# Performance work log

Hardware: AMD Instinct MI355X
Metric: run time of the kernel (lower is better)

## Reference

```python
import jax, jax.numpy as jnp
import numpy as np

E = 512   # embed_dim
H = 8     # num_heads
DH = E // H  # head_dim = 64
L = 1024  # tgt_len (language tokens)
S = 1024  # src_len (video/audio tokens)
B = 8     # batch
EPS = 1e-8


def setup_inputs() -> dict:
    key = jax.random.key(0)
    ks = jax.random.split(key, 12)
    xavier = float(np.sqrt(2.0 / (E + E)))
    inp = {
        "query": jax.random.normal(ks[0], (L, B, E), jnp.float32),
        "mod1": jax.random.normal(ks[1], (S, B, E), jnp.float32),
        "mod2": jax.random.normal(ks[2], (S, B, E), jnp.float32),
    }
    wnames = ["Wq", "Wk1", "Wk2", "Wv1", "Wv2", "Wg1", "Wg2", "Wo"]
    for i, n in enumerate(wnames):
        inp[n] = jax.random.normal(ks[3 + i], (E, E), jnp.float32) * xavier
        inp["b" + n[1:]] = jnp.zeros((E,), jnp.float32)
    return inp


def _heads(x):
    # (T, B, E) -> (B*H, T, DH), fairseq-style head split
    T = x.shape[0]
    return x.reshape(T, B * H, DH).transpose(1, 0, 2)


def reference(query, mod1, mod2,
              Wq, bq, Wk1, bk1, Wk2, bk2,
              Wv1, bv1, Wv2, bv2,
              Wg1, bg1, Wg2, bg2, Wo, bo):
    scaling = DH ** -0.5
    q = (query @ Wq.T + bq) * scaling          # (L, B, E)
    k1 = mod1 @ Wk1.T + bk1                    # (S, B, E)
    k2 = mod2 @ Wk2.T + bk2
    # gated values: v_i * sigmoid(gate_i(mod_i)), summed across modalities
    v = ((mod1 @ Wv1.T + bv1) * jax.nn.sigmoid(mod1 @ Wg1.T + bg1)
         + (mod2 @ Wv2.T + bv2) * jax.nn.sigmoid(mod2 @ Wg2.T + bg2))

    qh, k1h, k2h, vh = _heads(q), _heads(k1), _heads(k2), _heads(v)  # (B*H, T, DH)

    # 3x3 Gram determinant scores (computed via GEMMs, no [B,L,S,D] broadcast)
    ll = jnp.sum(qh * qh, -1)[:, :, None]        # (BH, L, 1)
    vv = jnp.sum(k1h * k1h, -1)[:, None, :]      # (BH, 1, S)
    aa = jnp.sum(k2h * k2h, -1)[:, None, :]
    va = jnp.sum(k1h * k2h, -1)[:, None, :]
    lv = jnp.einsum('bld,bsd->bls', qh, k1h)     # (BH, L, S)
    la = jnp.einsum('bld,bsd->bls', qh, k2h)
    det = (ll * (vv * aa - va * va)
           - lv * (lv * aa - la * va)
           + la * (lv * va - la * vv))
    scores = -jnp.sqrt(jnp.clip(det, EPS))       # (BH, L, S)

    attn = jax.nn.softmax(scores, axis=-1)
    out = jnp.einsum('bls,bsd->bld', attn, vh)   # (BH, L, DH)
    out = out.transpose(1, 0, 2).reshape(L, B, E)
    return out @ Wo.T + bo                       # (L, B, E)
```

## Files before the change

### kernel.cpp

```cpp
#include <hip/hip_runtime.h>
#include <math.h>


typedef short bf16x8 __attribute__((ext_vector_type(8)));
typedef float f32x4  __attribute__((ext_vector_type(4)));

#define MFMA16(a,b,c) __builtin_amdgcn_mfma_f32_16x16x32_bf16((a),(b),(c),0,0,0)

static constexpr float LOG2E_F = 1.4426950408889634f;
static constexpr float CBRT_L2E = 1.12994722f;
static constexpr float DEFER_THR = 11.54156033f;
static constexpr float EPS_SCALED = 2.0813689e-8f;

typedef const __attribute__((address_space(1))) unsigned int gas_u32;
typedef __attribute__((address_space(3))) unsigned int las_u32;

__device__ __forceinline__ void gload16(const void* g, void* l){
  __builtin_amdgcn_global_load_lds((gas_u32*)g, (las_u32*)l, 16, 0, 0);
}

__device__ __forceinline__ float b2f(unsigned short s){
  union { unsigned u; float f; } v; v.u = ((unsigned)s) << 16; return v.f;
}
__device__ __forceinline__ unsigned short f2b(float f){
  union { float f; unsigned u; } v; v.f = f;
  unsigned r = v.u + 0x7fffu + ((v.u >> 16) & 1u);
  return (unsigned short)(r >> 16);
}

__global__ __launch_bounds__(256) void cast3_kernel(
    const float* __restrict__ a, const float* __restrict__ b,
    const float* __restrict__ c, unsigned short* __restrict__ hi, int n)
{
  const int y = blockIdx.y;
  const float* src = (y == 0) ? a : ((y == 1) ? b : c);
  unsigned short* h = hi + (size_t)y * n;
  const int n8 = n >> 3;
  int stride = gridDim.x * 256;
  for (int i = blockIdx.x*256 + threadIdx.x; i < n8; i += stride){
    f32x4 v0 = *(const f32x4*)&src[i*8];
    f32x4 v1 = *(const f32x4*)&src[i*8 + 4];
    bf16x8 o;
    #pragma unroll
    for (int j = 0; j < 4; ++j){
      o[j]   = (short)f2b(v0[j]);
      o[j+4] = (short)f2b(v1[j]);
    }
    *(bf16x8*)&h[i*8] = o;
  }
}

__global__ __launch_bounds__(256) void splitW_kernel(
    const float* w0, const float* w1, const float* w2, const float* w3,
    const float* w4, const float* w5, const float* w6, const float* w7,
    unsigned short* __restrict__ hi, unsigned short* __restrict__ lo, int n)
{
  const int y = blockIdx.y;
  const float* src = w0;
  if (y == 1) src = w1; if (y == 2) src = w2; if (y == 3) src = w3;
  if (y == 4) src = w4; if (y == 5) src = w5; if (y == 6) src = w6;
  if (y == 7) src = w7;
  unsigned short* h = hi + (size_t)y * n;
  unsigned short* L = lo + (size_t)y * n;
  int stride = gridDim.x * 256;
  for (int i = blockIdx.x*256 + threadIdx.x; i < n; i += stride){
    float v = src[i];
    unsigned short hh = f2b(v);
    h[i] = hh;
    L[i] = f2b(v - b2f(hh));
  }
}

__global__ __launch_bounds__(256,3) void proj_qk_kernel(
    const unsigned short* __restrict__ xhi,
    const unsigned short* __restrict__ whi, const unsigned short* __restrict__ wlo,
    const float* __restrict__ bq, const float* __restrict__ bk1,
    const float* __restrict__ bk2,
    unsigned short* __restrict__ qh_hi, unsigned short* __restrict__ qh_lo,
    unsigned short* __restrict__ k1h_hi, unsigned short* __restrict__ k1h_lo,
    unsigned short* __restrict__ k2h_hi, unsigned short* __restrict__ k2h_lo)
{
  __shared__ unsigned short smem[2*3*4096];
  const int tid = threadIdx.x, w = tid >> 6, l = tid & 63;
  const int y = blockIdx.y, job = y >> 2;
  const int r0 = blockIdx.x * 128, e0 = (y & 3) * 128;
  const int lrow = l & 15, kg = l >> 4;

  const size_t NXs = (size_t)8192*512, NWs = (size_t)512*512;
  const unsigned short* Ahi = xhi + (size_t)job * NXs;
  const unsigned short* B1  = whi + (size_t)job * NWs;
  const unsigned short* B2  = wlo + (size_t)job * NWs;

  f32x4 acc[4][4];
  #pragma unroll
  for (int m = 0; m < 4; ++m)
    #pragma unroll
    for (int n = 0; n < 4; ++n) acc[m][n] = (f32x4){0.f,0.f,0.f,0.f};

  const int sgsw = ((l & 3) ^ ((l >> 3) & 3)) * 8;
  const int srA = r0 + w*16 + (l >> 2);
  const int srB = e0 + w*16 + (l >> 2);

  auto stage = [&](int buf, int kk){
    const int lb = buf*3*4096 + w*512;
    #pragma unroll
    for (int j = 0; j < 2; ++j){
      const size_t ga = (size_t)(srA + j*64)*512 + kk + sgsw;
      const size_t gb = (size_t)(srB + j*64)*512 + kk + sgsw;
      gload16(&Ahi[ga], &smem[lb + 0    + j*2048]);
      gload16(&B1[gb],  &smem[lb + 4096 + j*2048]);
      gload16(&B2[gb],  &smem[lb + 8192 + j*2048]);
    }
  };

  const int rowA = (w >> 1)*64 + lrow;
  const int rowB = (w & 1)*64 + lrow;
  const int kgs  = (kg ^ ((lrow >> 1) & 3)) * 8;

  auto compute = [&](int buf){
    const int bb = buf*3*4096;
    bf16x8 ah[4];
    #pragma unroll
    for (int m = 0; m < 4; ++m)
      ah[m] = *(const bf16x8*)&smem[bb + (rowA + m*16)*32 + kgs];
    #pragma unroll
    for (int n = 0; n < 4; ++n){
      const int rb = (rowB + n*16)*32 + kgs;
      bf16x8 b1 = *(const bf16x8*)&smem[bb + 4096 + rb];
      bf16x8 b2 = *(const bf16x8*)&smem[bb + 8192 + rb];
      #pragma unroll
      for (int m = 0; m < 4; ++m){
        acc[m][n] = MFMA16(ah[m], b1, acc[m][n]);
        acc[m][n] = MFMA16(ah[m], b2, acc[m][n]);
      }
    }
  };

  stage(0, 0);
  __syncthreads();
  for (int t = 0; t < 16; ++t){
    if (t < 15) stage((t+1) & 1, (t+1)*32);
    compute(t & 1);
    __syncthreads();
  }

  const float* bias = (job == 0) ? bq : ((job == 1) ? bk1 : bk2);
  const float scale = (job == 0) ? 0.125f*CBRT_L2E : CBRT_L2E;
  unsigned short* oH = (job == 0) ? qh_hi : ((job == 1) ? k1h_hi : k2h_hi);
  unsigned short* oL = (job == 0) ? qh_lo : ((job == 1) ? k1h_lo : k2h_lo);
  #pragma unroll
  for (int n = 0; n < 4; ++n){
    const int e = e0 + (w & 1)*64 + n*16 + lrow;
    const float bv = bias[e];
    #pragma unroll
    for (int m = 0; m < 4; ++m){
      #pragma unroll
      for (int q = 0; q < 4; ++q){
        const int r = r0 + (w >> 1)*64 + m*16 + kg*4 + q;
        const float yv = (acc[m][n][q] + bv) * scale;
        const int bh = ((r & 7) << 3) + (e >> 6);
        const size_t off = ((size_t)bh*1024 + (r >> 3))*64 + (e & 63);
        unsigned short hh = f2b(yv);
        oH[off] = hh;
        oL[off] = f2b(yv - b2f(hh));
      }
    }
  }
}

__global__ __launch_bounds__(256,2) void proj_vg_kernel(
    const unsigned short* __restrict__ xhi,
    const unsigned short* __restrict__ whi,
    const float* __restrict__ bv1, const float* __restrict__ bg1,
    const float* __restrict__ bv2, const float* __restrict__ bg2,
    float* __restrict__ vacc1, float* __restrict__ vacc2)
{
  __shared__ unsigned short smem[2*3*4096];
  const int tid = threadIdx.x, w = tid >> 6, l = tid & 63;
  const int y = blockIdx.y, job = 3 + (y >> 2);
  const int r0 = blockIdx.x * 128, e0 = (y & 3) * 128;
  const int lrow = l & 15, kg = l >> 4;

  const size_t NXs = (size_t)8192*512, NWs = (size_t)512*512;
  const unsigned short* Ahi = xhi + (size_t)(job - 2) * NXs;
  const unsigned short* B1  = whi + (size_t)((job == 3) ? 3 : 4) * NWs;
  const unsigned short* B2  = whi + (size_t)((job == 3) ? 5 : 6) * NWs;

  f32x4 acc[4][4], acc2[4][4];
  #pragma unroll
  for (int m = 0; m < 4; ++m)
    #pragma unroll
    for (int n = 0; n < 4; ++n){
      acc[m][n] = (f32x4){0.f,0.f,0.f,0.f};
      acc2[m][n] = (f32x4){0.f,0.f,0.f,0.f};
    }

  const int sgsw = ((l & 3) ^ ((l >> 3) & 3)) * 8;
  const int srA = r0 + w*16 + (l >> 2);
  const int srB = e0 + w*16 + (l >> 2);

  auto stage = [&](int buf, int kk){
    const int lb = buf*3*4096 + w*512;
    #pragma unroll
    for (int j = 0; j < 2; ++j){
      const size_t ga = (size_t)(srA + j*64)*512 + kk + sgsw;
      const size_t gb = (size_t)(srB + j*64)*512 + kk + sgsw;
      gload16(&Ahi[ga], &smem[lb + 0    + j*2048]);
      gload16(&B1[gb],  &smem[lb + 4096 + j*2048]);
      gload16(&B2[gb],  &smem[lb + 8192 + j*2048]);
    }
  };

  const int rowA = (w >> 1)*64 + lrow;
  const int rowB = (w & 1)*64 + lrow;
  const int kgs  = (kg ^ ((lrow >> 1) & 3)) * 8;

  auto compute = [&](int buf){
    const int bb = buf*3*4096;
    bf16x8 ah[4];
    #pragma unroll
    for (int m = 0; m < 4; ++m)
      ah[m] = *(const bf16x8*)&smem[bb + (rowA + m*16)*32 + kgs];
    #pragma unroll
    for (int n = 0; n < 4; ++n){
      const int rb = (rowB + n*16)*32 + kgs;
      bf16x8 b1 = *(const bf16x8*)&smem[bb + 4096 + rb];
      bf16x8 b2 = *(const bf16x8*)&smem[bb + 8192 + rb];
      #pragma unroll
      for (int m = 0; m < 4; ++m){
        acc[m][n]  = MFMA16(ah[m], b1, acc[m][n]);
        acc2[m][n] = MFMA16(ah[m], b2, acc2[m][n]);
      }
    }
  };

  stage(0, 0);
  __syncthreads();
  for (int t = 0; t < 16; ++t){
    if (t < 15) stage((t+1) & 1, (t+1)*32);
    compute(t & 1);
    __syncthreads();
  }

  const float* bvv = (job == 3) ? bv1 : bv2;
  const float* bgg = (job == 3) ? bg1 : bg2;
  float* outF = (job == 3) ? vacc1 : vacc2;
  #pragma unroll
  for (int n = 0; n < 4; ++n){
    const int e = e0 + (w & 1)*64 + n*16 + lrow;
    const float bv = bvv[e], bg_ = bgg[e];
    #pragma unroll
    for (int m = 0; m < 4; ++m){
      #pragma unroll
      for (int q = 0; q < 4; ++q){
        const int r = r0 + (w >> 1)*64 + m*16 + kg*4 + q;
        const float yv = acc[m][n][q] + bv;
        const float yg = acc2[m][n][q] + bg_;
        const float sg = 1.0f / (1.0f + exp2f(-yg * LOG2E_F));
        outF[(size_t)r*512 + e] = yv * sg;
      }
    }
  }
}

__global__ __launch_bounds__(256,2) void gemmout_kernel(
    const unsigned short* __restrict__ Ahi,
    const unsigned short* __restrict__ Bhi, const unsigned short* __restrict__ Blo,
    const float* __restrict__ bias, float* __restrict__ outF)
{
  __shared__ unsigned short smem[2*10240];
  const int tid = threadIdx.x, w = tid >> 6, l = tid & 63;
  const int r0 = blockIdx.x * 64, e0 = blockIdx.y * 128;
  const int lrow = l & 15, kg = l >> 4;

  f32x4 acc[2][4];
  #pragma unroll
  for (int m = 0; m < 2; ++m)
    #pragma unroll
    for (int n = 0; n < 4; ++n) acc[m][n] = (f32x4){0.f,0.f,0.f,0.f};

  const int sgsw = ((l & 3) ^ ((l >> 3) & 3)) * 8;
  const int srA = r0 + w*16 + (l >> 2);
  const int srB = e0 + w*16 + (l >> 2);

  auto stage = [&](int buf, int kk){
    const int lb = buf*10240;
    gload16(&Ahi[(size_t)srA*512 + kk + sgsw], &smem[lb + tid*8]);
    #pragma unroll
    for (int j = 0; j < 2; ++j){
      const size_t gb = (size_t)(srB + j*64)*512 + kk + sgsw;
      gload16(&Bhi[gb], &smem[lb + 2048 + (tid + j*256)*8]);
      gload16(&Blo[gb], &smem[lb + 6144 + (tid + j*256)*8]);
    }
  };

  const int rowA = (w >> 1)*32 + lrow;
  const int rowB = (w & 1)*64 + lrow;
  const int kgs  = (kg ^ ((lrow >> 1) & 3)) * 8;

  auto compute = [&](int buf){
    const int bb = buf*10240;
    bf16x8 ah[2];
    #pragma unroll
    for (int m = 0; m < 2; ++m)
      ah[m] = *(const bf16x8*)&smem[bb + (rowA + m*16)*32 + kgs];
    #pragma unroll
    for (int n = 0; n < 4; ++n){
      const int rb = (rowB + n*16)*32 + kgs;
      bf16x8 bh = *(const bf16x8*)&smem[bb + 2048 + rb];
      bf16x8 bl = *(const bf16x8*)&smem[bb + 6144 + rb];
      #pragma unroll
      for (int m = 0; m < 2; ++m){
        acc[m][n] = MFMA16(ah[m], bh, acc[m][n]);
        acc[m][n] = MFMA16(ah[m], bl, acc[m][n]);
      }
    }
  };

  stage(0, 0);
  __syncthreads();
  for (int t = 0; t < 16; ++t){
    if (t < 15) stage((t+1) & 1, (t+1)*32);
    compute(t & 1);
    __syncthreads();
  }

  #pragma unroll
  for (int n = 0; n < 4; ++n){
    const int e = e0 + (w & 1)*64 + n*16 + lrow;
    const float bv = bias[e];
    #pragma unroll
    for (int m = 0; m < 2; ++m){
      #pragma unroll
      for (int q = 0; q < 4; ++q){
        const int r = r0 + (w >> 1)*32 + m*16 + kg*4 + q;
        outF[(size_t)r*512 + e] = acc[m][n][q] + bv;
      }
    }
  }
}

__global__ __launch_bounds__(256) void norms_kernel(
    const unsigned short* __restrict__ qh, const unsigned short* __restrict__ ql,
    const unsigned short* __restrict__ k1h, const unsigned short* __restrict__ k1l,
    const unsigned short* __restrict__ k2h, const unsigned short* __restrict__ k2l,
    float* __restrict__ ll, f32x4* __restrict__ nrm4)
{
  const int idx = blockIdx.x*256 + threadIdx.x;
  const size_t base = (size_t)idx * 64;
  float sll = 0.f, svv = 0.f, saa = 0.f, sva = 0.f;
  #pragma unroll
  for (int j = 0; j < 8; ++j){
    bf16x8 q_h = *(const bf16x8*)&qh[base + j*8];
    bf16x8 q_l = *(const bf16x8*)&ql[base + j*8];
    bf16x8 a_h = *(const bf16x8*)&k1h[base + j*8];
    bf16x8 a_l = *(const bf16x8*)&k1l[base + j*8];
    bf16x8 c_h = *(const bf16x8*)&k2h[base + j*8];
    bf16x8 c_l = *(const bf16x8*)&k2l[base + j*8];
    #pragma unroll
    for (int i = 0; i < 8; ++i){
      float qv = b2f((unsigned short)q_h[i]) + b2f((unsigned short)q_l[i]);
      float a1 = b2f((unsigned short)a_h[i]) + b2f((unsigned short)a_l[i]);
      float a2 = b2f((unsigned short)c_h[i]) + b2f((unsigned short)c_l[i]);
      sll += qv*qv; svv += a1*a1; saa += a2*a2; sva += a1*a2;
    }
  }
  ll[idx] = sll;
  nrm4[idx] = (f32x4){svv*saa - sva*sva, saa, 2.0f*sva, svv};
}

__global__ __launch_bounds__(256) void vtrans_kernel(
    const float* __restrict__ v1, const float* __restrict__ v2,
    unsigned short* __restrict__ vTh)
{
  __shared__ unsigned short sH[64*64];
  const int bh = blockIdx.y, b = bh >> 3, h = bh & 7;
  const int s0 = blockIdx.x * 64;
  const int tid = threadIdx.x;
  for (int c = tid; c < 1024; c += 256){
    const int i = c >> 4, sl = c & 15;
    const size_t g = ((size_t)(s0 + i)*8 + b)*512 + h*64 + sl*4;
    f32x4 a = *(const f32x4*)&v1[g];
    f32x4 bb = *(const f32x4*)&v2[g];
    #pragma unroll
    for (int e = 0; e < 4; ++e)
      sH[(sl*4 + e)*64 + i] = f2b(a[e] + bb[e]);
  }
  __syncthreads();
  for (int c = tid; c < 512; c += 256){
    const int d = c >> 3, sl = c & 7;
    const size_t g = ((size_t)bh*64 + d)*1024 + s0 + sl*8;
    *(bf16x8*)&vTh[g] = *(const bf16x8*)&sH[d*64 + sl*8];
  }
}

__global__ __launch_bounds__(256,2) void attn_kernel(
    const unsigned short* __restrict__ qhh, const unsigned short* __restrict__ qhl,
    const unsigned short* __restrict__ k1hh, const unsigned short* __restrict__ k1hl,
    const unsigned short* __restrict__ k2hh, const unsigned short* __restrict__ k2hl,
    const unsigned short* __restrict__ vTh,
    const float* __restrict__ llv, const f32x4* __restrict__ nrm4,
    unsigned short* __restrict__ aoHi)
{
  __shared__ unsigned short sK1h[4096];
  __shared__ unsigned short sK1l[4096];
  __shared__ unsigned short sK2h[4096];
  __shared__ unsigned short sK2l[4096];
  __shared__ unsigned short sVh[4096];
  __shared__ unsigned short sPh[8192];
  __shared__ f32x4 sN4[64];

  const int bh = blockIdx.x & 63, l0 = (blockIdx.x >> 6) * 128;
  const int tid = threadIdx.x, w = tid >> 6, lane = tid & 63;
  const int lrow = lane & 15, kg = lane >> 4;

  bf16x8 qfh[2][2], qfl[2][2];
  #pragma unroll
  for (int m = 0; m < 2; ++m){
    const size_t qb = ((size_t)bh*1024 + l0 + w*32 + m*16 + lrow)*64 + kg*8;
    qfh[m][0] = *(const bf16x8*)&qhh[qb];
    qfl[m][0] = *(const bf16x8*)&qhl[qb];
    qfh[m][1] = *(const bf16x8*)&qhh[qb + 32];
    qfl[m][1] = *(const bf16x8*)&qhl[qb + 32];
  }
  float ll_r[2][4];
  #pragma unroll
  for (int m = 0; m < 2; ++m)
    #pragma unroll
    for (int q = 0; q < 4; ++q)
      ll_r[m][q] = llv[bh*1024 + l0 + w*32 + m*16 + kg*4 + q];

  f32x4 accO[2][4];
  #pragma unroll
  for (int m = 0; m < 2; ++m)
    #pragma unroll
    for (int i = 0; i < 4; ++i) accO[m][i] = (f32x4){0.f,0.f,0.f,0.f};
  float mn[2][4], s_run[2][4];
  #pragma unroll
  for (int m = 0; m < 2; ++m)
    #pragma unroll
    for (int q = 0; q < 4; ++q){ mn[m][q] = 1e30f; s_run[m][q] = 0.f; }

  const int c0 = tid, c1 = tid + 256;
  const int r0g = c0 >> 3, g0 = ((c0 & 7) ^ (r0g & 7)) * 8;
  const int r1g = c1 >> 3, g1 = ((c1 & 7) ^ (r1g & 7)) * 8;

  for (int ss = 0; ss < 1024; ss += 64){
    {
      const size_t kb = (size_t)bh*1024 + ss;
      const size_t k0 = (kb + r0g)*64 + g0;
      const size_t k1_ = (kb + r1g)*64 + g1;
      gload16(&k1hh[k0], &sK1h[c0*8]);  gload16(&k1hh[k1_], &sK1h[c1*8]);
      gload16(&k1hl[k0], &sK1l[c0*8]);  gload16(&k1hl[k1_], &sK1l[c1*8]);
      gload16(&k2hh[k0], &sK2h[c0*8]);  gload16(&k2hh[k1_], &sK2h[c1*8]);
      gload16(&k2hl[k0], &sK2l[c0*8]);  gload16(&k2hl[k1_], &sK2l[c1*8]);
      const size_t v0 = ((size_t)bh*64 + r0g)*1024 + ss + g0;
      const size_t v1 = ((size_t)bh*64 + r1g)*1024 + ss + g1;
      gload16(&vTh[v0], &sVh[c0*8]);    gload16(&vTh[v1], &sVh[c1*8]);
      if (tid < 64) gload16(&nrm4[(size_t)bh*1024 + ss + tid], &sN4[tid]);
    }
    __syncthreads();

    float p_[2][4][4];
    float tmn[2][4];
    #pragma unroll
    for (int m = 0; m < 2; ++m)
      #pragma unroll
      for (int q = 0; q < 4; ++q) tmn[m][q] = 1e30f;

    #pragma unroll
    for (int nt = 0; nt < 4; ++nt){
      f32x4 lv[2], la[2];
      #pragma unroll
      for (int m = 0; m < 2; ++m){ lv[m] = (f32x4){0.f,0.f,0.f,0.f}; la[m] = (f32x4){0.f,0.f,0.f,0.f}; }
      __builtin_amdgcn_s_setprio(1);
      #pragma unroll
      for (int ks = 0; ks < 2; ++ks){
        const int row = nt*16 + lrow;
        const int off = row*64 + (((ks*4 + kg) ^ (row & 7)) * 8);
        bf16x8 b1h = *(const bf16x8*)&sK1h[off];
        bf16x8 b1l = *(const bf16x8*)&sK1l[off];
        bf16x8 b2h = *(const bf16x8*)&sK2h[off];
        bf16x8 b2l = *(const bf16x8*)&sK2l[off];
        #pragma unroll
        for (int m = 0; m < 2; ++m){
          lv[m] = MFMA16(qfh[m][ks], b1h, lv[m]);
          lv[m] = MFMA16(qfh[m][ks], b1l, lv[m]);
          lv[m] = MFMA16(qfl[m][ks], b1h, lv[m]);
          la[m] = MFMA16(qfh[m][ks], b2h, la[m]);
          la[m] = MFMA16(qfh[m][ks], b2l, la[m]);
          la[m] = MFMA16(qfl[m][ks], b2h, la[m]);
        }
      }
      __builtin_amdgcn_s_setprio(0);
      f32x4 n4 = sN4[nt*16 + lrow];
      const float cross = n4[0], c_aa = n4[1], c_va2 = n4[2], c_vv = n4[3];
      #pragma unroll
      for (int m = 0; m < 2; ++m){
        #pragma unroll
        for (int q = 0; q < 4; ++q){
          const float flv = lv[m][q], fla = la[m][q];
          float t = fmaf(-c_vv, fla*fla, (flv*fla)*c_va2);
          t = fmaf(-c_aa, flv*flv, t);
          const float det = fmaf(ll_r[m][q], cross, t);
          const float sq = __builtin_amdgcn_sqrtf(fmaxf(det, EPS_SCALED));
          p_[m][nt][q] = sq;
          tmn[m][q] = fminf(tmn[m][q], sq);
        }
      }
    }
    #pragma unroll
    for (int m = 0; m < 2; ++m)
      #pragma unroll
      for (int q = 0; q < 4; ++q){
        tmn[m][q] = fminf(tmn[m][q], __shfl_xor(tmn[m][q], 1));
        tmn[m][q] = fminf(tmn[m][q], __shfl_xor(tmn[m][q], 2));
        tmn[m][q] = fminf(tmn[m][q], __shfl_xor(tmn[m][q], 4));
        tmn[m][q] = fminf(tmn[m][q], __shfl_xor(tmn[m][q], 8));
      }
    int up = 0;
    #pragma unroll
    for (int m = 0; m < 2; ++m)
      #pragma unroll
      for (int q = 0; q < 4; ++q) up |= (tmn[m][q] < mn[m][q] - DEFER_THR) ? 1 : 0;
    if (__any(up)){
      #pragma unroll
      for (int m = 0; m < 2; ++m)
        #pragma unroll
        for (int q = 0; q < 4; ++q){
          const float mnn = fminf(mn[m][q], tmn[m][q]);
          const float rs = __builtin_amdgcn_exp2f(mnn - mn[m][q]);
          mn[m][q] = mnn;
          s_run[m][q] *= rs;
          #pragma unroll
          for (int dt = 0; dt < 4; ++dt) accO[m][dt][q] *= rs;
        }
    }
    float ps[2][4];
    #pragma unroll
    for (int m = 0; m < 2; ++m)
      #pragma unroll
      for (int q = 0; q < 4; ++q) ps[m][q] = 0.f;
    #pragma unroll
    for (int nt = 0; nt < 4; ++nt)
      #pragma unroll
      for (int m = 0; m < 2; ++m)
        #pragma unroll
        for (int q = 0; q < 4; ++q){
          const float e = __builtin_amdgcn_exp2f(mn[m][q] - p_[m][nt][q]);
          p_[m][nt][q] = e;
          ps[m][q] += e;
        }
    #pragma unroll
    for (int m = 0; m < 2; ++m)
      #pragma unroll
      for (int q = 0; q < 4; ++q){
        float v = ps[m][q];
        v += __shfl_xor(v, 1); v += __shfl_xor(v, 2);
        v += __shfl_xor(v, 4); v += __shfl_xor(v, 8);
        s_run[m][q] += v;
      }

    #pragma unroll
    for (int m = 0; m < 2; ++m){
      #pragma unroll
      for (int nt = 0; nt < 4; ++nt){
        const int col = nt*16 + lrow;
        const int cg = col >> 3, cr = col & 7;
        #pragma unroll
        for (int qp = 0; qp < 2; ++qp){
          unsigned int pk;
          asm("v_cvt_pk_bf16_f32 %0, %1, %2" : "=v"(pk)
              : "v"(p_[m][nt][qp*2]), "v"(p_[m][nt][qp*2+1]));
          const int ra = m*16 + kg*4 + qp*2, rb = ra + 1;
          sPh[w*2048 + ra*64 + ((cg ^ (ra & 7))*8) + cr] = (unsigned short)(pk & 0xffffu);
          sPh[w*2048 + rb*64 + ((cg ^ (rb & 7))*8) + cr] = (unsigned short)(pk >> 16);
        }
      }
    }

    __builtin_amdgcn_s_setprio(1);
    #pragma unroll
    for (int ks = 0; ks < 2; ++ks){
      bf16x8 pa[2];
      #pragma unroll
      for (int m = 0; m < 2; ++m){
        const int prow = m*16 + lrow;
        pa[m] = *(const bf16x8*)&sPh[w*2048 + prow*64 + (((ks*4 + kg) ^ (prow & 7))*8)];
      }
      #pragma unroll
      for (int dt = 0; dt < 4; ++dt){
        const int vrow = dt*16 + lrow;
        bf16x8 bvh = *(const bf16x8*)&sVh[vrow*64 + (((ks*4 + kg) ^ (vrow & 7))*8)];
        #pragma unroll
        for (int m = 0; m < 2; ++m)
          accO[m][dt] = MFMA16(pa[m], bvh, accO[m][dt]);
      }
    }
    __builtin_amdgcn_s_setprio(0);
    __syncthreads();
  }

  const int b = bh >> 3, h = bh & 7;
  #pragma unroll
  for (int m = 0; m < 2; ++m){
    float rcp[4];
    #pragma unroll
    for (int q = 0; q < 4; ++q) rcp[q] = __builtin_amdgcn_rcpf(s_run[m][q]);
    #pragma unroll
    for (int dt = 0; dt < 4; ++dt){
      const int d = dt*16 + lrow;
      #pragma unroll
      for (int q = 0; q < 4; ++q){
        const int l_ = l0 + w*32 + m*16 + kg*4 + q;
        aoHi[((size_t)l_*8 + b)*512 + h*64 + d] = f2b(accO[m][dt][q] * rcp[q]);
      }
    }
  }
}

extern "C" void kernel_launch(void* const* d_in, const int* in_sizes, int n_in,
                              void* d_out, int out_size, void* d_ws, size_t ws_size,
                              hipStream_t stream)
{
  const float* query = (const float*)d_in[0];
  const float* mod1  = (const float*)d_in[1];
  const float* mod2  = (const float*)d_in[2];
  const float* bq  = (const float*)d_in[4];
  const float* bk1 = (const float*)d_in[6];
  const float* bk2 = (const float*)d_in[8];
  const float* bv1 = (const float*)d_in[10];
  const float* bv2 = (const float*)d_in[12];
  const float* bg1 = (const float*)d_in[14];
  const float* bg2 = (const float*)d_in[16];
  const float* bo  = (const float*)d_in[18];

  char* p = (char*)d_ws;
  auto take = [&](size_t bytes) -> char* {
    char* r = p; p += (bytes + 255) & ~(size_t)255; return r;
  };
  const size_t NX = (size_t)8192*512;
  const size_t NW = (size_t)512*512;
  const size_t XB = NX*2, WB = NW*2;
  const size_t HB = (size_t)64*1024*64*2;
  const size_t FB = NX*4;
  const size_t NB = (size_t)64*1024*4;

  unsigned short* xhi = (unsigned short*)take(3*XB);
  unsigned short* whi = (unsigned short*)take(8*WB);
  unsigned short* wlo = (unsigned short*)take(8*WB);
  unsigned short* qh_hi  = (unsigned short*)take(HB);
  unsigned short* qh_lo  = (unsigned short*)take(HB);
  unsigned short* k1h_hi = (unsigned short*)take(HB);
  unsigned short* k1h_lo = (unsigned short*)take(HB);
  unsigned short* k2h_hi = (unsigned short*)take(HB);
  unsigned short* k2h_lo = (unsigned short*)take(HB);
  unsigned short* vT_hi  = (unsigned short*)take(HB);
  float* vacc1 = (float*)take(FB);
  float* vacc2 = (float*)take(FB);
  unsigned short* ao_hi = (unsigned short*)take(HB);
  float* llv = (float*)take(NB);
  f32x4* nrm4 = (f32x4*)take(4*NB);

  cast3_kernel<<<dim3(2048,3), 256, 0, stream>>>(query, mod1, mod2, xhi, (int)NX);
  splitW_kernel<<<dim3(256,8), 256, 0, stream>>>(
      (const float*)d_in[3], (const float*)d_in[5], (const float*)d_in[7],
      (const float*)d_in[9], (const float*)d_in[11], (const float*)d_in[13],
      (const float*)d_in[15], (const float*)d_in[17], whi, wlo, (int)NW);

  proj_qk_kernel<<<dim3(64, 12), 256, 0, stream>>>(
      xhi, whi, wlo, bq, bk1, bk2,
      qh_hi, qh_lo, k1h_hi, k1h_lo, k2h_hi, k2h_lo);
  proj_vg_kernel<<<dim3(64, 8), 256, 0, stream>>>(
      xhi, whi, bv1, bg1, bv2, bg2, vacc1, vacc2);

  norms_kernel<<<256, 256, 0, stream>>>(qh_hi, qh_lo, k1h_hi, k1h_lo,
                                        k2h_hi, k2h_lo, llv, nrm4);
  vtrans_kernel<<<dim3(16, 64), 256, 0, stream>>>(vacc1, vacc2, vT_hi);

  attn_kernel<<<512, 256, 0, stream>>>(
      qh_hi, qh_lo, k1h_hi, k1h_lo, k2h_hi, k2h_lo, vT_hi,
      llv, nrm4, ao_hi);

  gemmout_kernel<<<dim3(128, 4), 256, 0, stream>>>(
      ao_hi, whi + 7*NW, wlo + 7*NW, bo, (float*)d_out);
}
```

Measured before the change: 349.9 us.

## Fuse prep kernels, write transposed bf16 V, and register-prefetch K/V tiles in attention

The cast and weight-split kernels are merged into one launch, and the norms and V-sum kernels are merged into another. The V/gate projection now writes a bf16 transposed V directly, so the fp32 intermediate and the transpose pass go away. The attention kernel prefetches the next K/V tile into registers while computing the current one, then writes it to LDS after the compute. The per-column norms are now read directly from global memory instead of LDS. This aims to cut launch overhead and intermediate traffic and to hide load latency. The costs are higher register pressure, an extra barrier per tile, scattered 2-byte transposed stores, and a double bf16 rounding of V.

```diff
diff --git a/kernel.cpp b/kernel.cpp
--- a/kernel.cpp
+++ b/kernel.cpp
@@ -4,6 +4,8 @@
 
 typedef short bf16x8 __attribute__((ext_vector_type(8)));
 typedef float f32x4  __attribute__((ext_vector_type(4)));
+typedef unsigned int u32x4 __attribute__((ext_vector_type(4)));
+typedef unsigned short u16x4 __attribute__((ext_vector_type(4)));
 
 #define MFMA16(a,b,c) __builtin_amdgcn_mfma_f32_16x16x32_bf16((a),(b),(c),0,0,0)
 
@@ -28,46 +30,46 @@
   return (unsigned short)(r >> 16);
 }
 
-__global__ __launch_bounds__(256) void cast3_kernel(
-    const float* __restrict__ a, const float* __restrict__ b,
-    const float* __restrict__ c, unsigned short* __restrict__ hi, int n)
+__global__ __launch_bounds__(256) void prep_kernel(
+    const float* __restrict__ xq, const float* __restrict__ x1,
+    const float* __restrict__ x2,
+    const float* w0, const float* w1, const float* w2, const float* w3,
+    const float* w4, const float* w5, const float* w6, const float* w7,
+    unsigned short* __restrict__ xhi,
+    unsigned short* __restrict__ whi, unsigned short* __restrict__ wlo)
 {
-  const int y = blockIdx.y;
-  const float* src = (y == 0) ? a : ((y == 1) ? b : c);
-  unsigned short* h = hi + (size_t)y * n;
-  const int n8 = n >> 3;
-  int stride = gridDim.x * 256;
-  for (int i = blockIdx.x*256 + threadIdx.x; i < n8; i += stride){
-    f32x4 v0 = *(const f32x4*)&src[i*8];
-    f32x4 v1 = *(const f32x4*)&src[i*8 + 4];
+  const int blk = blockIdx.x, tid = threadIdx.x;
+  const size_t NX = (size_t)8192*512, NW = (size_t)512*512;
+  if (blk < 6144){
+    const int y = blk >> 11;
+    const int i = ((blk & 2047)*256 + tid);
+    const float* src = (y == 0) ? xq : ((y == 1) ? x1 : x2);
+    f32x4 v0 = *(const f32x4*)&src[(size_t)i*8];
+    f32x4 v1 = *(const f32x4*)&src[(size_t)i*8 + 4];
     bf16x8 o;
     #pragma unroll
     for (int j = 0; j < 4; ++j){
       o[j]   = (short)f2b(v0[j]);
       o[j+4] = (short)f2b(v1[j]);
     }
-    *(bf16x8*)&h[i*8] = o;
-  }
-}
-
-__global__ __launch_bounds__(256) void splitW_kernel(
-    const float* w0, const float* w1, const float* w2, const float* w3,
-    const float* w4, const float* w5, const float* w6, const float* w7,
-    unsigned short* __restrict__ hi, unsigned short* __restrict__ lo, int n)
-{
-  const int y = blockIdx.y;
-  const float* src = w0;
-  if (y == 1) src = w1; if (y == 2) src = w2; if (y == 3) src = w3;
-  if (y == 4) src = w4; if (y == 5) src = w5; if (y == 6) src = w6;
-  if (y == 7) src = w7;
-  unsigned short* h = hi + (size_t)y * n;
-  unsigned short* L = lo + (size_t)y * n;
-  int stride = gridDim.x * 256;
-  for (int i = blockIdx.x*256 + threadIdx.x; i < n; i += stride){
-    float v = src[i];
-    unsigned short hh = f2b(v);
-    h[i] = hh;
-    L[i] = f2b(v - b2f(hh));
+    *(bf16x8*)&xhi[(size_t)y*NX + (size_t)i*8] = o;
+  } else {
+    const int y = (blk - 6144) >> 8;
+    const int t = ((blk - 6144) & 255)*256 + tid;
+    const float* src = w0;
+    if (y == 1) src = w1; if (y == 2) src = w2; if (y == 3) src = w3;
+    if (y == 4) src = w4; if (y == 5) src = w5; if (y == 6) src = w6;
+    if (y == 7) src = w7;
+    f32x4 v = *(const f32x4*)&src[(size_t)t*4];
+    u16x4 hh, ll_;
+    #pragma unroll
+    for (int j = 0; j < 4; ++j){
+      unsigned short h = f2b(v[j]);
+      hh[j] = h;
+      ll_[j] = f2b(v[j] - b2f(h));
+    }
+    *(u16x4*)&whi[(size_t)y*NW + (size_t)t*4] = hh;
+    *(u16x4*)&wlo[(size_t)y*NW + (size_t)t*4] = ll_;
   }
 }
 
@@ -173,7 +175,7 @@
     const unsigned short* __restrict__ whi,
     const float* __restrict__ bv1, const float* __restrict__ bg1,
     const float* __restrict__ bv2, const float* __restrict__ bg2,
-    float* __restrict__ vacc1, float* __restrict__ vacc2)
+    unsigned short* __restrict__ vT1, unsigned short* __restrict__ vT2)
 {
   __shared__ unsigned short smem[2*3*4096];
   const int tid = threadIdx.x, w = tid >> 6, l = tid & 63;
@@ -244,11 +246,12 @@
 
   const float* bvv = (job == 3) ? bv1 : bv2;
   const float* bgg = (job == 3) ? bg1 : bg2;
-  float* outF = (job == 3) ? vacc1 : vacc2;
+  unsigned short* vTp = (job == 3) ? vT1 : vT2;
   #pragma unroll
   for (int n = 0; n < 4; ++n){
     const int e = e0 + (w & 1)*64 + n*16 + lrow;
     const float bv = bvv[e], bg_ = bgg[e];
+    const int h_ = e >> 6, d_ = e & 63;
     #pragma unroll
     for (int m = 0; m < 4; ++m){
       #pragma unroll
@@ -257,7 +260,8 @@
         const float yv = acc[m][n][q] + bv;
         const float yg = acc2[m][n][q] + bg_;
         const float sg = 1.0f / (1.0f + exp2f(-yg * LOG2E_F));
-        outF[(size_t)r*512 + e] = yv * sg;
+        const int b_ = r & 7, t_ = r >> 3;
+        vTp[((size_t)((b_ << 3) + h_)*64 + d_)*1024 + t_] = f2b(yv * sg);
       }
     }
   }
@@ -340,57 +344,46 @@
   }
 }
 
-__global__ __launch_bounds__(256) void norms_kernel(
+__global__ __launch_bounds__(256) void post_kernel(
     const unsigned short* __restrict__ qh, const unsigned short* __restrict__ ql,
     const unsigned short* __restrict__ k1h, const unsigned short* __restrict__ k1l,
     const unsigned short* __restrict__ k2h, const unsigned short* __restrict__ k2l,
-    float* __restrict__ ll, f32x4* __restrict__ nrm4)
+    float* __restrict__ ll, f32x4* __restrict__ nrm4,
+    const unsigned short* __restrict__ vT1, const unsigned short* __restrict__ vT2,
+    unsigned short* __restrict__ vT)
 {
-  const int idx = blockIdx.x*256 + threadIdx.x;
-  const size_t base = (size_t)idx * 64;
-  float sll = 0.f, svv = 0.f, saa = 0.f, sva = 0.f;
-  #pragma unroll
-  for (int j = 0; j < 8; ++j){
-    bf16x8 q_h = *(const bf16x8*)&qh[base + j*8];
-    bf16x8 q_l = *(const bf16x8*)&ql[base + j*8];
-    bf16x8 a_h = *(const bf16x8*)&k1h[base + j*8];
-    bf16x8 a_l = *(const bf16x8*)&k1l[base + j*8];
-    bf16x8 c_h = *(const bf16x8*)&k2h[base + j*8];
-    bf16x8 c_l = *(const bf16x8*)&k2l[base + j*8];
-    #pragma unroll
-    for (int i = 0; i < 8; ++i){
-      float qv = b2f((unsigned short)q_h[i]) + b2f((unsigned short)q_l[i]);
-      float a1 = b2f((unsigned short)a_h[i]) + b2f((unsigned short)a_l[i]);
-      float a2 = b2f((unsigned short)c_h[i]) + b2f((unsigned short)c_l[i]);
-      sll += qv*qv; svv += a1*a1; saa += a2*a2; sva += a1*a2;
-    }
-  }
-  ll[idx] = sll;
-  nrm4[idx] = (f32x4){svv*saa - sva*sva, saa, 2.0f*sva, svv};
-}
-
-__global__ __launch_bounds__(256) void vtrans_kernel(
-    const float* __restrict__ v1, const float* __restrict__ v2,
-    unsigned short* __restrict__ vTh)
-{
-  __shared__ unsigned short sH[64*64];
-  const int bh = blockIdx.y, b = bh >> 3, h = bh & 7;
-  const int s0 = blockIdx.x * 64;
-  const int tid = threadIdx.x;
-  for (int c = tid; c < 1024; c += 256){
-    const int i = c >> 4, sl = c & 15;
-    const size_t g = ((size_t)(s0 + i)*8 + b)*512 + h*64 + sl*4;
-    f32x4 a = *(const f32x4*)&v1[g];
-    f32x4 bb = *(const f32x4*)&v2[g];
-    #pragma unroll
-    for (int e = 0; e < 4; ++e)
-      sH[(sl*4 + e)*64 + i] = f2b(a[e] + bb[e]);
-  }
-  __syncthreads();
-  for (int c = tid; c < 512; c += 256){
-    const int d = c >> 3, sl = c & 7;
-    const size_t g = ((size_t)bh*64 + d)*1024 + s0 + sl*8;
-    *(bf16x8*)&vTh[g] = *(const bf16x8*)&sH[d*64 + sl*8];
+  const int blk = blockIdx.x, tid = threadIdx.x;
+  if (blk < 256){
+    const int idx = blk*256 + tid;
+    const size_t base = (size_t)idx * 64;
+    float sll = 0.f, svv = 0.f, saa = 0.f, sva = 0.f;
+    #pragma unroll
+    for (int j = 0; j < 8; ++j){
+      bf16x8 q_h = *(const bf16x8*)&qh[base + j*8];
+      bf16x8 q_l = *(const bf16x8*)&ql[base + j*8];
+      bf16x8 a_h = *(const bf16x8*)&k1h[base + j*8];
+      bf16x8 a_l = *(const bf16x8*)&k1l[base + j*8];
+      bf16x8 c_h = *(const bf16x8*)&k2h[base + j*8];
+      bf16x8 c_l = *(const bf16x8*)&k2l[base + j*8];
+      #pragma unroll
+      for (int i = 0; i < 8; ++i){
+        float qv = b2f((unsigned short)q_h[i]) + b2f((unsigned short)q_l[i]);
+        float a1 = b2f((unsigned short)a_h[i]) + b2f((unsigned short)a_l[i]);
+        float a2 = b2f((unsigned short)c_h[i]) + b2f((unsigned short)c_l[i]);
+        sll += qv*qv; svv += a1*a1; saa += a2*a2; sva += a1*a2;
+      }
+    }
+    ll[idx] = sll;
+    nrm4[idx] = (f32x4){svv*saa - sva*sva, saa, 2.0f*sva, svv};
+  } else {
+    const size_t i = ((size_t)(blk - 256)*256 + tid) * 8;
+    bf16x8 a = *(const bf16x8*)&vT1[i];
+    bf16x8 b = *(const bf16x8*)&vT2[i];
+    bf16x8 o;
+    #pragma unroll
+    for (int j = 0; j < 8; ++j)
+      o[j] = (short)f2b(b2f((unsigned short)a[j]) + b2f((unsigned short)b[j]));
+    *(bf16x8*)&vT[i] = o;
   }
 }
 
@@ -408,7 +401,6 @@
   __shared__ unsigned short sK2l[4096];
   __shared__ unsigned short sVh[4096];
   __shared__ unsigned short sPh[8192];
-  __shared__ f32x4 sN4[64];
 
   const int bh = blockIdx.x & 63, l0 = (blockIdx.x >> 6) * 128;
   const int tid = threadIdx.x, w = tid >> 6, lane = tid & 63;
@@ -445,21 +437,33 @@
   const int r0g = c0 >> 3, g0 = ((c0 & 7) ^ (r0g & 7)) * 8;
   const int r1g = c1 >> 3, g1 = ((c1 & 7) ^ (r1g & 7)) * 8;
 
+  u32x4 st0,st1,st2,st3,st4,st5,st6,st7,st8,st9;
+  auto LOADREGS = [&](int ss2){
+    const size_t kb = (size_t)bh*1024 + ss2;
+    const size_t k0 = (kb + r0g)*64 + g0;
+    const size_t k1_ = (kb + r1g)*64 + g1;
+    st0 = *(const u32x4*)&k1hh[k0];  st1 = *(const u32x4*)&k1hh[k1_];
+    st2 = *(const u32x4*)&k1hl[k0];  st3 = *(const u32x4*)&k1hl[k1_];
+    st4 = *(const u32x4*)&k2hh[k0];  st5 = *(const u32x4*)&k2hh[k1_];
+    st6 = *(const u32x4*)&k2hl[k0];  st7 = *(const u32x4*)&k2hl[k1_];
+    const size_t v0 = ((size_t)bh*64 + r0g)*1024 + ss2 + g0;
+    const size_t v1 = ((size_t)bh*64 + r1g)*1024 + ss2 + g1;
+    st8 = *(const u32x4*)&vTh[v0];   st9 = *(const u32x4*)&vTh[v1];
+  };
+  auto WRITELDS = [&](){
+    *(u32x4*)&sK1h[c0*8] = st0;  *(u32x4*)&sK1h[c1*8] = st1;
+    *(u32x4*)&sK1l[c0*8] = st2;  *(u32x4*)&sK1l[c1*8] = st3;
+    *(u32x4*)&sK2h[c0*8] = st4;  *(u32x4*)&sK2h[c1*8] = st5;
+    *(u32x4*)&sK2l[c0*8] = st6;  *(u32x4*)&sK2l[c1*8] = st7;
+    *(u32x4*)&sVh[c0*8]  = st8;  *(u32x4*)&sVh[c1*8]  = st9;
+  };
+
+  LOADREGS(0);
+  WRITELDS();
+  __syncthreads();
+
   for (int ss = 0; ss < 1024; ss += 64){
-    {
-      const size_t kb = (size_t)bh*1024 + ss;
-      const size_t k0 = (kb + r0g)*64 + g0;
-      const size_t k1_ = (kb + r1g)*64 + g1;
-      gload16(&k1hh[k0], &sK1h[c0*8]);  gload16(&k1hh[k1_], &sK1h[c1*8]);
-      gload16(&k1hl[k0], &sK1l[c0*8]);  gload16(&k1hl[k1_], &sK1l[c1*8]);
-      gload16(&k2hh[k0], &sK2h[c0*8]);  gload16(&k2hh[k1_], &sK2h[c1*8]);
-      gload16(&k2hl[k0], &sK2l[c0*8]);  gload16(&k2hl[k1_], &sK2l[c1*8]);
-      const size_t v0 = ((size_t)bh*64 + r0g)*1024 + ss + g0;
-      const size_t v1 = ((size_t)bh*64 + r1g)*1024 + ss + g1;
-      gload16(&vTh[v0], &sVh[c0*8]);    gload16(&vTh[v1], &sVh[c1*8]);
-      if (tid < 64) gload16(&nrm4[(size_t)bh*1024 + ss + tid], &sN4[tid]);
-    }
-    __syncthreads();
+    if (ss + 64 < 1024) LOADREGS(ss + 64);
 
     float p_[2][4][4];
     float tmn[2][4];
@@ -493,7 +497,7 @@
         }
       }
       __builtin_amdgcn_s_setprio(0);
-      f32x4 n4 = sN4[nt*16 + lrow];
+      f32x4 n4 = *(const f32x4*)&nrm4[(size_t)bh*1024 + ss + nt*16 + lrow];
       const float cross = n4[0], c_aa = n4[1], c_va2 = n4[2], c_vv = n4[3];
       #pragma unroll
       for (int m = 0; m < 2; ++m){
@@ -598,7 +602,12 @@
       }
     }
     __builtin_amdgcn_s_setprio(0);
+
     __syncthreads();
+    if (ss + 64 < 1024){
+      WRITELDS();
+      __syncthreads();
+    }
   }
 
   const int b = bh >> 3, h = bh & 7;
@@ -643,7 +652,6 @@
   const size_t NW = (size_t)512*512;
   const size_t XB = NX*2, WB = NW*2;
   const size_t HB = (size_t)64*1024*64*2;
-  const size_t FB = NX*4;
   const size_t NB = (size_t)64*1024*4;
 
   unsigned short* xhi = (unsigned short*)take(3*XB);
@@ -655,31 +663,31 @@
   unsigned short* k1h_lo = (unsigned short*)take(HB);
   unsigned short* k2h_hi = (unsigned short*)take(HB);
   unsigned short* k2h_lo = (unsigned short*)take(HB);
-  unsigned short* vT_hi  = (unsigned short*)take(HB);
-  float* vacc1 = (float*)take(FB);
-  float* vacc2 = (float*)take(FB);
+  unsigned short* vT1 = (unsigned short*)take(HB);
+  unsigned short* vT2 = (unsigned short*)take(HB);
+  unsigned short* vT  = (unsigned short*)take(HB);
   unsigned short* ao_hi = (unsigned short*)take(HB);
   float* llv = (float*)take(NB);
   f32x4* nrm4 = (f32x4*)take(4*NB);
 
-  cast3_kernel<<<dim3(2048,3), 256, 0, stream>>>(query, mod1, mod2, xhi, (int)NX);
-  splitW_kernel<<<dim3(256,8), 256, 0, stream>>>(
+  prep_kernel<<<8192, 256, 0, stream>>>(
+      query, mod1, mod2,
       (const float*)d_in[3], (const float*)d_in[5], (const float*)d_in[7],
       (const float*)d_in[9], (const float*)d_in[11], (const float*)d_in[13],
-      (const float*)d_in[15], (const float*)d_in[17], whi, wlo, (int)NW);
+      (const float*)d_in[15], (const float*)d_in[17], xhi, whi, wlo);
 
   proj_qk_kernel<<<dim3(64, 12), 256, 0, stream>>>(
       xhi, whi, wlo, bq, bk1, bk2,
       qh_hi, qh_lo, k1h_hi, k1h_lo, k2h_hi, k2h_lo);
   proj_vg_kernel<<<dim3(64, 8), 256, 0, stream>>>(
-      xhi, whi, bv1, bg1, bv2, bg2, vacc1, vacc2);
-
-  norms_kernel<<<256, 256, 0, stream>>>(qh_hi, qh_lo, k1h_hi, k1h_lo,
-                                        k2h_hi, k2h_lo, llv, nrm4);
-  vtrans_kernel<<<dim3(16, 64), 256, 0, stream>>>(vacc1, vacc2, vT_hi);
+      xhi, whi, bv1, bg1, bv2, bg2, vT1, vT2);
+
+  post_kernel<<<2304, 256, 0, stream>>>(
+      qh_hi, qh_lo, k1h_hi, k1h_lo, k2h_hi, k2h_lo,
+      llv, nrm4, vT1, vT2, vT);
 
   attn_kernel<<<512, 256, 0, stream>>>(
-      qh_hi, qh_lo, k1h_hi, k1h_lo, k2h_hi, k2h_lo, vT_hi,
+      qh_hi, qh_lo, k1h_hi, k1h_lo, k2h_hi, k2h_lo, vT,
       llv, nrm4, ao_hi);
 
   gemmout_kernel<<<dim3(128, 4), 256, 0, stream>>>(
```

Measured after the change: 376.3 us. 1.08x slower.
